# Kernel tuning notes

Hardware: AMD Instinct MI355X
Metric: run time of the kernel (lower is better)

## Reference

```python
import jax, jax.numpy as jnp
import numpy as np
from itertools import combinations

NUM_ENT = 7
DIM_ENT = 256
REL_HIDDEN = 256
HIDDEN = 1024
BATCH = 16384
PAIRS = np.array(list(combinations(range(NUM_ENT), 2)), dtype=np.int32)  # [21, 2]


def setup_inputs() -> dict:
    key = jax.random.key(0)
    k1, k2, k3 = jax.random.split(key, 3)
    ctx = jax.random.normal(k1, (BATCH, NUM_ENT * DIM_ENT), dtype=jnp.float32)
    # torch init: uniform(-init_range, init_range) weights, zero bias
    W_rel = jax.random.uniform(k2, (2 * DIM_ENT, REL_HIDDEN), dtype=jnp.float32, minval=-0.01, maxval=0.01)
    b_rel = jnp.zeros((REL_HIDDEN,), dtype=jnp.float32)
    W_fc = jax.random.uniform(k3, (NUM_ENT * DIM_ENT + REL_HIDDEN, HIDDEN), dtype=jnp.float32, minval=-0.01, maxval=0.01)
    b_fc = jnp.zeros((HIDDEN,), dtype=jnp.float32)
    return {"ctx": ctx, "W_rel": W_rel, "b_rel": b_rel, "W_fc": W_fc, "b_fc": b_fc}


def reference(ctx, W_rel, b_rel, W_fc, b_fc):
    B = ctx.shape[0]
    ents = ctx.reshape(B, NUM_ENT, DIM_ENT)
    idx_i = jnp.asarray(PAIRS[:, 0])
    idx_j = jnp.asarray(PAIRS[:, 1])
    # gather both endpoints of each of the 21 pairs: [B, 21, 2*DIM_ENT]
    pair_feat = jnp.concatenate([ents[:, idx_i, :], ents[:, idx_j, :]], axis=-1)
    # batched small Linear + Tanh: [B, 21, REL_HIDDEN]
    rel = jnp.tanh(jnp.einsum("bpe,eh->bph", pair_feat, W_rel) + b_rel)
    # faithful replication of torch: cat pair-major then view(B, rel_hidden, -1).sum(2)
    rel = rel.reshape(B, 21 * REL_HIDDEN).reshape(B, REL_HIDDEN, 21).sum(axis=2)
    inpt = jnp.concatenate([ctx, rel], axis=1)  # [B, input_size]
    # dropout output is discarded in the original forward (no-op); fc1 uses inpt
    out = jnp.tanh(inpt @ W_fc + b_fc)
    return out[None, :, :]  # [1, B, HIDDEN]
```

## Files before the change

### kernel.cpp

```cpp
#include <hip/hip_runtime.h>

typedef unsigned short u16;
typedef __attribute__((ext_vector_type(8))) short short8;
typedef __attribute__((ext_vector_type(4))) float f32x4;
typedef const __attribute__((address_space(1))) unsigned int g_u32;
typedef __attribute__((address_space(3))) unsigned int l_u32;

#define BATCH 16384
#define XCOLS 2048

__device__ __forceinline__ void gload16(const void* g, void* l) {
  __builtin_amdgcn_global_load_lds((g_u32*)g, (l_u32*)l, 16, 0, 0);
}
__device__ __forceinline__ u16 f2bf(float f) {
  unsigned int x = __builtin_bit_cast(unsigned int, f);
  x += 0x7fffu + ((x >> 16) & 1u);
  return (u16)(x >> 16);
}
__device__ __forceinline__ float bf2f(u16 u) {
  return __builtin_bit_cast(float, (unsigned int)u << 16);
}
__device__ __forceinline__ int swz(int P) { return P ^ (((P >> 7) & 7) << 4); }

__device__ __forceinline__ float fast_tanh(float x) {
  float e2 = __expf(2.0f * x);
  return 1.0f - 2.0f * __builtin_amdgcn_rcpf(e2 + 1.0f);
}

__device__ const unsigned char PI[21] = {0,0,0,0,0,0,1,1,1,1,1,2,2,2,2,3,3,3,4,4,5};
__device__ const unsigned char PJ[21] = {1,2,3,4,5,6,2,3,4,5,6,3,4,5,6,4,5,6,5,6,6};

__global__ void prep_ctx(const float* __restrict__ ctx, u16* __restrict__ X) {
  const int total = BATCH * 224;
  for (int u = blockIdx.x * blockDim.x + threadIdx.x; u < total;
       u += gridDim.x * blockDim.x) {
    int b = u / 224, c8 = u - b * 224;
    const float4* s = (const float4*)(ctx + (size_t)b * 1792 + c8 * 8);
    float4 v0 = s[0], v1 = s[1];
    short8 o;
    o[0] = (short)f2bf(v0.x); o[1] = (short)f2bf(v0.y);
    o[2] = (short)f2bf(v0.z); o[3] = (short)f2bf(v0.w);
    o[4] = (short)f2bf(v1.x); o[5] = (short)f2bf(v1.y);
    o[6] = (short)f2bf(v1.z); o[7] = (short)f2bf(v1.w);
    *(short8*)(X + (size_t)b * XCOLS + c8 * 8) = o;
  }
}

__global__ void prep_wrel(const float* __restrict__ Wr, u16* __restrict__ WcT) {
  int idx = blockIdx.x * 256 + threadIdx.x;
  if (idx >= 512 * 256) return;
  int n = idx >> 8, k = idx & 255;
  float v = (n < 256) ? Wr[k * 256 + n] : Wr[(256 + k) * 256 + (n - 256)];
  WcT[idx] = f2bf(v);
}

__global__ void prep_wfc(const float* __restrict__ W, u16* __restrict__ WT) {
  __shared__ float t[64][65];
  int k0 = blockIdx.x * 64;
  int n0 = blockIdx.y * 64;
  int tx = threadIdx.x & 63, ty = threadIdx.x >> 6;
  #pragma unroll
  for (int i = 0; i < 64; i += 4)
    t[ty + i][tx] = W[(size_t)(k0 + ty + i) * 1024 + n0 + tx];
  __syncthreads();
  #pragma unroll
  for (int i = 0; i < 64; i += 4) {
    int n = ty + i;
    WT[(size_t)(n0 + n) * XCOLS + k0 + tx] = f2bf(t[tx][n]);
  }
}

__global__ __launch_bounds__(512, 4) void gemm1_fused(u16* __restrict__ X, const u16* __restrict__ WcT,
                                                      const float* __restrict__ b_rel) {
  __shared__ __align__(16) u16 smem[36864];
  char* sb = (char*)smem;
  const int tid = threadIdx.x;
  const int wid = tid >> 6, lane = tid & 63;
  const int b_base = blockIdx.x * 8;
  float brl[4];
  #pragma unroll
  for (int n = 0; n < 4; ++n)
    brl[n] = 0.5f * b_rel[(wid & 3) * 64 + n * 16 + (lane & 15)];
  f32x4 acc[4][4] = {};
  for (int kt = 0; kt < 4; ++kt) {
    const int kb = kt * 64;
    {
      int L = swz(tid * 16);
      int row = L >> 7, koff = (L & 127) >> 1;
      int r = row < 56 ? row : 55;
      int bl = r / 7, e = r - bl * 7;
      gload16(X + (size_t)(b_base + bl) * XCOLS + e * 256 + kb + koff, sb + wid * 1024);
    }
    #pragma unroll
    for (int i = 0; i < 8; ++i) {
      int slot = i * 512 + tid;
      int L = swz(slot * 16);
      int rn = L >> 7, koff = (L & 127) >> 1;
      gload16(WcT + rn * 256 + kb + koff, sb + 8192 + (i * 512 + wid * 64) * 16);
    }
    __syncthreads();
    #pragma unroll
    for (int kk = 0; kk < 64; kk += 32) {
      short8 a[4], b[4];
      #pragma unroll
      for (int m = 0; m < 4; ++m) {
        int row = m * 16 + (lane & 15);
        int L = row * 128 + kk * 2 + ((lane >> 4) << 4);
        a[m] = *(const short8*)(sb + swz(L));
      }
      #pragma unroll
      for (int n = 0; n < 4; ++n) {
        int rn = wid * 64 + n * 16 + (lane & 15);
        int L = rn * 128 + kk * 2 + ((lane >> 4) << 4);
        b[n] = *(const short8*)(sb + 8192 + swz(L));
      }
      #pragma unroll
      for (int m = 0; m < 4; ++m)
        #pragma unroll
        for (int n = 0; n < 4; ++n)
          acc[m][n] = __builtin_amdgcn_mfma_f32_16x16x32_bf16(a[m], b[n], acc[m][n], 0, 0, 0);
    }
    __syncthreads();
  }
  for (int rd = 0; rd < 4; ++rd) {
    const int rbase = rd * 14;
    #pragma unroll
    for (int m = 0; m < 4; ++m) {
      int row0 = m * 16 + ((lane >> 4) << 2);
      #pragma unroll
      for (int v = 0; v < 4; ++v) {
        int lr = row0 + v - rbase;
        if (lr >= 0 && lr < 14) {
          #pragma unroll
          for (int n = 0; n < 4; ++n) {
            int col = wid * 64 + n * 16 + (lane & 15);
            int L = lr * 1024 + col * 2;
            *(u16*)(sb + (L ^ ((lr & 7) << 4))) = f2bf(acc[m][n][v] + brl[n]);
          }
        }
      }
    }
    __syncthreads();
    for (int i = tid; i < 1344; i += 512) {
      int bb = i >= 672;
      int rem = i - bb * 672;
      int k8 = rem * 8;
      int p = k8 >> 8, h = k8 & 255;
      int li = bb * 7 + PI[p], lj = bb * 7 + PJ[p];
      int Lu = li * 1024 + h * 2;
      int Lv = lj * 1024 + 512 + h * 2;
      short8 uu = *(const short8*)(sb + (Lu ^ ((li & 7) << 4)));
      short8 vv = *(const short8*)(sb + (Lv ^ ((lj & 7) << 4)));
      float t[8];
      #pragma unroll
      for (int e = 0; e < 8; ++e)
        t[e] = fast_tanh(bf2f((u16)uu[e]) + bf2f((u16)vv[e]));
      f32x4* T = (f32x4*)(sb + 14336 + bb * 21504 + k8 * 4);
      T[0] = f32x4{t[0], t[1], t[2], t[3]};
      T[1] = f32x4{t[4], t[5], t[6], t[7]};
    }
    __syncthreads();
    {
      int bb = tid >> 8, r = tid & 255;
      const float* T = (const float*)(sb + 14336 + bb * 21504);
      float s = 0.f;
      #pragma unroll
      for (int c = 0; c < 21; ++c) s += T[r * 21 + c];
      X[(size_t)(b_base + rd * 2 + bb) * XCOLS + 1792 + r] = f2bf(s);
    }
    __syncthreads();
  }
}

__global__ __launch_bounds__(256, 3) void gemm2(const u16* __restrict__ X, const u16* __restrict__ WT,
                                                const float* __restrict__ b_fc, float* __restrict__ out) {
  __shared__ __align__(16) u16 smem[16384];
  char* sb = (char*)smem;
  const int tid = threadIdx.x;
  const int wid = tid >> 6, lane = tid & 63;
  const int wr = wid >> 1, wc = wid & 1;
  int bid = blockIdx.x;
  int sw = (bid & 7) * 128 + (bid >> 3);
  int bm = sw >> 3, bn = sw & 7;
  const size_t mBase = (size_t)bm * 128;
  const int nBase = bn * 128;
  f32x4 acc[4][4] = {};
  for (int kt = 0; kt < 32; ++kt) {
    const int kb = kt * 64;
    #pragma unroll
    for (int i = 0; i < 4; ++i) {
      int cb = (wid + i * 4) * 64;
      int L = swz((cb + lane) * 16);
      int row = L >> 7, koff = (L & 127) >> 1;
      gload16(X + (mBase + row) * XCOLS + kb + koff, sb + cb * 16);
      gload16(WT + (size_t)(nBase + row) * XCOLS + kb + koff, sb + 16384 + cb * 16);
    }
    __syncthreads();
    #pragma unroll
    for (int kk = 0; kk < 64; kk += 32) {
      short8 a[4], b[4];
      #pragma unroll
      for (int m = 0; m < 4; ++m) {
        int row = wr * 64 + m * 16 + (lane & 15);
        int L = row * 128 + kk * 2 + ((lane >> 4) << 4);
        a[m] = *(const short8*)(sb + swz(L));
      }
      #pragma unroll
      for (int n = 0; n < 4; ++n) {
        int rn = wc * 64 + n * 16 + (lane & 15);
        int L = rn * 128 + kk * 2 + ((lane >> 4) << 4);
        b[n] = *(const short8*)(sb + 16384 + swz(L));
      }
      #pragma unroll
      for (int m = 0; m < 4; ++m)
        #pragma unroll
        for (int n = 0; n < 4; ++n)
          acc[m][n] = __builtin_amdgcn_mfma_f32_16x16x32_bf16(a[m], b[n], acc[m][n], 0, 0, 0);
    }
    __syncthreads();
  }
  #pragma unroll
  for (int m = 0; m < 4; ++m) {
    int row0 = wr * 64 + m * 16 + ((lane >> 4) << 2);
    #pragma unroll
    for (int n = 0; n < 4; ++n) {
      int col = nBase + wc * 64 + n * 16 + (lane & 15);
      float bias = b_fc[col];
      #pragma unroll
      for (int v = 0; v < 4; ++v)
        out[(mBase + row0 + v) * 1024 + col] = fast_tanh(acc[m][n][v] + bias);
    }
  }
}

extern "C" void kernel_launch(void* const* d_in, const int* in_sizes, int n_in,
                              void* d_out, int out_size, void* d_ws, size_t ws_size,
                              hipStream_t stream) {
  const float* ctx   = (const float*)d_in[0];
  const float* W_rel = (const float*)d_in[1];
  const float* b_rel = (const float*)d_in[2];
  const float* W_fc  = (const float*)d_in[3];
  const float* b_fc  = (const float*)d_in[4];
  float* out = (float*)d_out;
  u16* X    = (u16*)d_ws;
  u16* WcT  = X + (size_t)BATCH * XCOLS;
  u16* WfcT = WcT + 512 * 256;
  prep_ctx<<<2048, 256, 0, stream>>>(ctx, X);
  prep_wrel<<<512, 256, 0, stream>>>(W_rel, WcT);
  prep_wfc<<<dim3(32, 16), 256, 0, stream>>>(W_fc, WfcT);
  gemm1_fused<<<2048, 512, 0, stream>>>(X, WcT, b_rel);
  gemm2<<<1024, 256, 0, stream>>>(X, WfcT, b_fc, out);
}
```

Measured before the change: 201.4 us.

## Restructure relation epilogue: fp32 transposed MFMA output, LDS atomic pair-sum reduction

The gemm1 epilogue now swaps MFMA operands so each lane holds four consecutive hidden columns and writes them as fp32 vectors into LDS. The per-pair tanh terms are accumulated straight into a per-batch relation buffer with LDS atomicAdd, replacing the bf16 staging, the tanh table and the serial 21-term sum. Batches are processed in two rounds instead of four, and pair indices come from packed octal constants rather than a device-memory table. This removes synchronisation passes and intermediate stores, but adds LDS atomic contention, and the change only touches the smaller of the two GEMMs.

New measurement: 319.5 us. 58.6% more time.

```diff
diff --git a/kernel.cpp b/kernel.cpp
--- a/kernel.cpp
+++ b/kernel.cpp
@@ -1,8 +1,10 @@
 #include <hip/hip_runtime.h>
 
 typedef unsigned short u16;
+typedef unsigned int u32;
 typedef __attribute__((ext_vector_type(8))) short short8;
 typedef __attribute__((ext_vector_type(4))) float f32x4;
+typedef __attribute__((ext_vector_type(2))) u32 u32x2;
 typedef const __attribute__((address_space(1))) unsigned int g_u32;
 typedef __attribute__((address_space(3))) unsigned int l_u32;
 
@@ -13,22 +15,19 @@
   __builtin_amdgcn_global_load_lds((g_u32*)g, (l_u32*)l, 16, 0, 0);
 }
 __device__ __forceinline__ u16 f2bf(float f) {
-  unsigned int x = __builtin_bit_cast(unsigned int, f);
+  u32 x = __builtin_bit_cast(u32, f);
   x += 0x7fffu + ((x >> 16) & 1u);
   return (u16)(x >> 16);
 }
-__device__ __forceinline__ float bf2f(u16 u) {
-  return __builtin_bit_cast(float, (unsigned int)u << 16);
-}
 __device__ __forceinline__ int swz(int P) { return P ^ (((P >> 7) & 7) << 4); }
 
 __device__ __forceinline__ float fast_tanh(float x) {
-  float e2 = __expf(2.0f * x);
-  return 1.0f - 2.0f * __builtin_amdgcn_rcpf(e2 + 1.0f);
-}
-
-__device__ const unsigned char PI[21] = {0,0,0,0,0,0,1,1,1,1,1,2,2,2,2,3,3,3,4,4,5};
-__device__ const unsigned char PJ[21] = {1,2,3,4,5,6,2,3,4,5,6,3,4,5,6,4,5,6,5,6,6};
+  float e = __builtin_amdgcn_exp2f(x * 2.885390081777927f);
+  return __builtin_fmaf(-2.0f, __builtin_amdgcn_rcpf(e + 1.0f), 1.0f);
+}
+
+#define PIPK 0544333222211111000000ULL
+#define PJPK 0665654654365432654321ULL
 
 __global__ void prep_ctx(const float* __restrict__ ctx, u16* __restrict__ X) {
   const int total = BATCH * 224;
@@ -74,13 +73,16 @@
                                                       const float* __restrict__ b_rel) {
   __shared__ __align__(16) u16 smem[36864];
   char* sb = (char*)smem;
+  float* relbuf = (float*)(sb + 57344);
   const int tid = threadIdx.x;
   const int wid = tid >> 6, lane = tid & 63;
   const int b_base = blockIdx.x * 8;
-  float brl[4];
-  #pragma unroll
-  for (int n = 0; n < 4; ++n)
-    brl[n] = 0.5f * b_rel[(wid & 3) * 64 + n * 16 + (lane & 15)];
+  f32x4 bias[4] = {};
+  if (wid < 4) {
+    #pragma unroll
+    for (int n = 0; n < 4; ++n)
+      bias[n] = *(const f32x4*)(b_rel + wid * 64 + n * 16 + ((lane >> 4) << 2));
+  }
   f32x4 acc[4][4] = {};
   for (int kt = 0; kt < 4; ++kt) {
     const int kb = kt * 64;
@@ -118,57 +120,64 @@
       for (int m = 0; m < 4; ++m)
         #pragma unroll
         for (int n = 0; n < 4; ++n)
-          acc[m][n] = __builtin_amdgcn_mfma_f32_16x16x32_bf16(a[m], b[n], acc[m][n], 0, 0, 0);
-    }
-    __syncthreads();
-  }
-  for (int rd = 0; rd < 4; ++rd) {
-    const int rbase = rd * 14;
+          acc[m][n] = __builtin_amdgcn_mfma_f32_16x16x32_bf16(b[n], a[m], acc[m][n], 0, 0, 0);
+    }
+    __syncthreads();
+  }
+  *(f32x4*)(sb + 57344 + tid * 16) = f32x4{0.f, 0.f, 0.f, 0.f};
+  for (int rd = 0; rd < 2; ++rd) {
+    const int rbase = rd * 28;
     #pragma unroll
     for (int m = 0; m < 4; ++m) {
-      int row0 = m * 16 + ((lane >> 4) << 2);
-      #pragma unroll
-      for (int v = 0; v < 4; ++v) {
-        int lr = row0 + v - rbase;
-        if (lr >= 0 && lr < 14) {
-          #pragma unroll
-          for (int n = 0; n < 4; ++n) {
-            int col = wid * 64 + n * 16 + (lane & 15);
-            int L = lr * 1024 + col * 2;
-            *(u16*)(sb + (L ^ ((lr & 7) << 4))) = f2bf(acc[m][n][v] + brl[n]);
-          }
+      int row = m * 16 + (lane & 15);
+      int lr = row - rbase;
+      if (lr >= 0 && lr < 28) {
+        #pragma unroll
+        for (int n = 0; n < 4; ++n) {
+          f32x4 val = acc[m][n] + bias[n];
+          int h0 = wid * 64 + n * 16 + ((lane >> 4) << 2);
+          int L = lr * 2048 + h0 * 4;
+          *(f32x4*)(sb + (L ^ ((lr & 7) << 4))) = val;
         }
       }
     }
     __syncthreads();
-    for (int i = tid; i < 1344; i += 512) {
-      int bb = i >= 672;
-      int rem = i - bb * 672;
-      int k8 = rem * 8;
-      int p = k8 >> 8, h = k8 & 255;
-      int li = bb * 7 + PI[p], lj = bb * 7 + PJ[p];
-      int Lu = li * 1024 + h * 2;
-      int Lv = lj * 1024 + 512 + h * 2;
-      short8 uu = *(const short8*)(sb + (Lu ^ ((li & 7) << 4)));
-      short8 vv = *(const short8*)(sb + (Lv ^ ((lj & 7) << 4)));
-      float t[8];
-      #pragma unroll
-      for (int e = 0; e < 8; ++e)
-        t[e] = fast_tanh(bf2f((u16)uu[e]) + bf2f((u16)vv[e]));
-      f32x4* T = (f32x4*)(sb + 14336 + bb * 21504 + k8 * 4);
-      T[0] = f32x4{t[0], t[1], t[2], t[3]};
-      T[1] = f32x4{t[4], t[5], t[6], t[7]};
-    }
-    __syncthreads();
-    {
-      int bb = tid >> 8, r = tid & 255;
-      const float* T = (const float*)(sb + 14336 + bb * 21504);
-      float s = 0.f;
-      #pragma unroll
-      for (int c = 0; c < 21; ++c) s += T[r * 21 + c];
-      X[(size_t)(b_base + rd * 2 + bb) * XCOLS + 1792 + r] = f2bf(s);
-    }
-    __syncthreads();
+    for (u32 i = tid; i < 5376; i += 512) {
+      u32 bb = i / 1344;
+      u32 rem = i - bb * 1344;
+      u32 k4 = rem << 2;
+      u32 p = k4 >> 8, h0 = k4 & 255;
+      int pi = (int)((PIPK >> (3 * p)) & 7);
+      int pj = (int)((PJPK >> (3 * p)) & 7);
+      int li = (int)bb * 7 + pi, lj = (int)bb * 7 + pj;
+      int Lu = (li * 2048 + (int)h0 * 4) ^ ((li & 7) << 4);
+      int Lv = (lj * 2048 + 1024 + (int)h0 * 4) ^ ((lj & 7) << 4);
+      f32x4 uu = *(const f32x4*)(sb + Lu);
+      f32x4 vv = *(const f32x4*)(sb + Lv);
+      float t0 = fast_tanh(uu[0] + vv[0]);
+      float t1 = fast_tanh(uu[1] + vv[1]);
+      float t2 = fast_tanh(uu[2] + vv[2]);
+      float t3 = fast_tanh(uu[3] + vv[3]);
+      u32 r0 = k4 / 21;
+      int s = (int)(r0 * 21 + 21 - k4);
+      float p0 = t0 + (s > 1 ? t1 : 0.f) + (s > 2 ? t2 : 0.f) + (s > 3 ? t3 : 0.f);
+      int gb = rd * 4 + (int)bb;
+      atomicAdd(&relbuf[gb * 256 + (int)r0], p0);
+      if (s < 4) {
+        float p1 = (s <= 1 ? t1 : 0.f) + (s <= 2 ? t2 : 0.f) + (s <= 3 ? t3 : 0.f);
+        atomicAdd(&relbuf[gb * 256 + (int)r0 + 1], p1);
+      }
+    }
+    __syncthreads();
+  }
+  {
+    int o = tid * 4;
+    int gb = o >> 8, r = o & 255;
+    f32x4 s4 = *(const f32x4*)(sb + 57344 + o * 4);
+    u32x2 w;
+    w[0] = (u32)f2bf(s4[0]) | ((u32)f2bf(s4[1]) << 16);
+    w[1] = (u32)f2bf(s4[2]) | ((u32)f2bf(s4[3]) << 16);
+    *(u32x2*)(X + (size_t)(b_base + gb) * XCOLS + 1792 + r) = w;
   }
 }
 
```
